# Optimization experiments

Hardware: AMD Instinct MI355X
Metric: run time of the kernel (lower is better)

## Reference

```python
import jax, jax.numpy as jnp
import numpy as np

N, G, MAX_N, E, H = 20000, 200, 100, 320000, 4
F_IN, NHID, NCLS = 128, 128, 10
DQ = 2 * NHID   # pooling-stack input dim = 2*nhid
K1 = 25         # ceil(0.25 * avg_num_nodes)


def _lin(key, fi, fo):
    kw, kb = jax.random.split(key)
    s = 1.0 / np.sqrt(fi)
    return (jax.random.uniform(kw, (fi, fo), jnp.float32, -s, s),
            jax.random.uniform(kb, (fo,), jnp.float32, -s, s))


def setup_inputs():
    key = jax.random.key(0)
    ks = jax.random.split(key, 32)
    x = jax.random.normal(ks[0], (N, F_IN), jnp.float32)
    gid = jax.random.randint(ks[1], (E,), 0, G)
    u = jax.random.randint(ks[2], (E,), 0, MAX_N)
    v = jax.random.randint(ks[3], (E,), 0, MAX_N)
    edge_index = jnp.stack([gid * MAX_N + u, gid * MAX_N + v]).astype(jnp.int32)
    batch = (jnp.arange(N) // MAX_N).astype(jnp.int32)
    d = {}
    d['x'], d['edge_index'], d['batch'] = x, edge_index, batch
    d['W1'], d['b1'] = _lin(ks[4], F_IN, NHID)
    d['W2'], d['b2'] = _lin(ks[5], NHID, NHID)
    d['S0'] = jax.random.normal(ks[6], (1, K1, DQ), jnp.float32) * (1.0 / np.sqrt(DQ))
    d['Wq0'], d['bq0'] = _lin(ks[7], DQ, DQ)
    d['Wk0'], d['bk0'] = _lin(ks[8], DQ, DQ)
    d['Wv0'], d['bv0'] = _lin(ks[9], DQ, DQ)
    d['Wo0'], d['bo0'] = _lin(ks[10], DQ, DQ)
    d['Wq1'], d['bq1'] = _lin(ks[11], DQ, NHID)
    d['Wk1'], d['bk1'] = _lin(ks[12], DQ, NHID)
    d['Wv1'], d['bv1'] = _lin(ks[13], DQ, NHID)
    d['Wo1'], d['bo1'] = _lin(ks[14], NHID, NHID)
    d['S2'] = jax.random.normal(ks[15], (1, 1, NHID), jnp.float32) * (1.0 / np.sqrt(NHID))
    d['Wq2'], d['bq2'] = _lin(ks[16], NHID, NHID)
    d['Wk2'], d['bk2'] = _lin(ks[17], NHID, NHID)
    d['Wv2'], d['bv2'] = _lin(ks[18], NHID, NHID)
    d['Wo2'], d['bo2'] = _lin(ks[19], NHID, NHID)
    d['Wl'], d['bl'] = _lin(ks[20], NHID, NHID)
    d['Wc1'], d['bc1'] = _lin(ks[21], NHID, NHID)
    d['Wc2'], d['bc2'] = _lin(ks[22], NHID, NHID // 2)
    d['Wc3'], d['bc3'] = _lin(ks[23], NHID // 2, NCLS)
    return d


def gcn(h, src, dst, W, b):
    # PyG GCNConv: add self loops, sym-normalize, scatter-add, bias
    h = h @ W
    loop = jnp.arange(N, dtype=src.dtype)
    s = jnp.concatenate([src, loop])
    t = jnp.concatenate([dst, loop])
    deg = jax.ops.segment_sum(jnp.ones(s.shape[0], h.dtype), t, num_segments=N)
    dinv = jax.lax.rsqrt(jnp.maximum(deg, 1.0))
    norm = (dinv[s] * dinv[t])[:, None]
    return jax.ops.segment_sum(h[s] * norm, t, num_segments=N) + b


def to_dense(v, batch):
    counts = jax.ops.segment_sum(jnp.ones(v.shape[0], jnp.int32), batch, num_segments=G)
    start = jnp.cumsum(counts) - counts
    pos = jnp.arange(v.shape[0]) - start[batch]
    dense = jnp.zeros((G, MAX_N, v.shape[1]), v.dtype).at[batch, pos].set(v)
    mask = jnp.zeros((G, MAX_N), bool).at[batch, pos].set(True)
    return dense, mask


def attn_block(Q, K, V, Wo, bo, mask_bias):
    # MAB core with cluster=True: softmax over the QUERY (seed) axis, ln=False
    B, nq, dv = Q.shape
    dh = dv // H
    Qh = Q.reshape(B, nq, H, dh)
    Kh = K.reshape(B, K.shape[1], H, dh)
    Vh = V.reshape(B, V.shape[1], H, dh)
    score = jnp.einsum('bqhd,bkhd->bhqk', Qh, Kh) / jnp.sqrt(jnp.float32(dv))
    if mask_bias is not None:
        score = score + mask_bias[:, None, None, :]
    A = jax.nn.softmax(score, axis=2)  # cluster assignment over seeds
    O = Q + jnp.einsum('bhqk,bkhd->bqhd', A, Vh).reshape(B, nq, dv)
    return O + jax.nn.relu(O @ Wo + bo)


def reference(x, edge_index, batch, W1, b1, W2, b2, S0, Wq0, bq0, Wk0, bk0, Wv0, bv0, Wo0, bo0,
              Wq1, bq1, Wk1, bk1, Wv1, bv1, Wo1, bo1, S2, Wq2, bq2, Wk2, bk2, Wv2, bv2, Wo2, bo2,
              Wl, bl, Wc1, bc1, Wc2, bc2, Wc3, bc3):
    src, dst = edge_index[0], edge_index[1]
    x1 = jax.nn.relu(gcn(x, src, dst, W1, b1))
    x2 = jax.nn.relu(gcn(x1, src, dst, W2, b2))
    p1 = jax.ops.segment_sum(x1, batch, num_segments=G)  # global_add_pool
    p2 = jax.ops.segment_sum(x2, batch, num_segments=G)
    xcat = jnp.concatenate([x1, x2], axis=1)             # [N, 2*nhid]
    dense, mask = to_dense(xcat, batch)
    mask_bias = (1.0 - mask.astype(jnp.float32)) * -1e9
    # --- GMPool_G: PMA with GCNConv for K/V on the node graph ---
    Kd, _ = to_dense(gcn(xcat, src, dst, Wk0, bk0), batch)
    Vd, _ = to_dense(gcn(xcat, src, dst, Wv0, bv0), batch)
    Q0 = jnp.broadcast_to(S0, (G, K1, DQ)) @ Wq0 + bq0
    O0 = attn_block(Q0, Kd, Vd, Wo0, bo0, mask_bias)     # [G, 25, 256]
    # --- SelfAtt (SAB), mask consumed above ---
    Q1 = O0 @ Wq1 + bq1
    K1d = O0 @ Wk1 + bk1
    V1d = O0 @ Wv1 + bv1
    O1 = attn_block(Q1, K1d, V1d, Wo1, bo1, None)        # [G, 25, 128]
    # --- GMPool_I: PMA with 1 seed ---
    Q2 = jnp.broadcast_to(S2, (G, 1, NHID)) @ Wq2 + bq2
    K2d = O1 @ Wk2 + bk2
    V2d = O1 @ Wv2 + bv2
    O2 = attn_block(Q2, K2d, V2d, Wo2, bo2, None)        # [G, 1, 128]
    z = (O2 @ Wl + bl)[:, 0, :]
    z = jax.nn.relu(z @ Wc1 + bc1)                        # dropout = identity at eval
    z = jax.nn.relu(z @ Wc2 + bc2)
    logits = z @ Wc3 + bc3
    return (logits, p1, p2)
```

## Files before the change

### kernel.cpp

```cpp
#include <hip/hip_runtime.h>
#include <hip/hip_bf16.h>
#include <cstdint>
#include <cstddef>

typedef __hip_bfloat16 bf16;
typedef __attribute__((ext_vector_type(8))) short s16x8;
typedef __attribute__((ext_vector_type(4))) float f32x4;

#define MAXN 100
#define HH   4
#define FIN  128
#define KS1  25
#define GLDK 136

static inline int ceil_div(int a, int b){ return (a + b - 1) / b; }

__device__ inline short f2bf(float f){
  unsigned int u = __float_as_uint(f);
  u = (u + 0x7FFF + ((u >> 16) & 1)) >> 16;
  return (short)u;
}
__device__ inline float loadf(const void* s, size_t i, bool isbf){
  return isbf ? __bfloat162float(((const bf16*)s)[i]) : ((const float*)s)[i];
}
__device__ inline bool block_sniff(const void* x, int tid, int* flagS){
  if (tid < 64){
    unsigned short b = ((const unsigned short*)x)[2 * tid];
    float v = __uint_as_float(((unsigned)b) << 16);
    float a = fabsf(v);
    bool ok = (a >= 6.1e-5f && a <= 16384.f);
    unsigned long long m = __ballot(ok);
    if (tid == 0) *flagS = (__popcll(m) >= 32) ? 1 : 0;
  }
  __syncthreads();
  return *flagS != 0;
}

struct PrepBatch {
  const void* src[40];
  void*       dst[40];
  int         a[40];
  int         b[40];
  int         blk0[41];
  int         ne;
  const void* xptr;
};

__global__ __launch_bounds__(256) void prep_all(PrepBatch pb){
  __shared__ int flagS;
  __shared__ short T[64][66];
  int tid = threadIdx.x;
  bool isbf = block_sniff(pb.xptr, tid, &flagS);
  int blk = blockIdx.x;
  int t = 0;
  while (t + 1 < pb.ne && pb.blk0[t + 1] <= blk) t++;
  int local = blk - pb.blk0[t];
  const void* s = pb.src[t];
  int bt = pb.b[t];
  if (bt < 0){
    float val = (bt == -2) ? 1.0f : 0.0f;
    int n = pb.a[t];
    float* d = (float*)pb.dst[t];
    int v = local * 256 + tid;
    int base = v * 4;
    if (base + 3 < n) ((float4*)d)[v] = make_float4(val, val, val, val);
    else for (int j = base; j < n && j < base + 4; j++) d[j] = val;
  } else if (bt == 0){
    int n = pb.a[t];
    float* d = (float*)pb.dst[t];
    int v = local * 256 + tid;
    int base = v * 4;
    if (base + 3 < n){
      float4 f;
      if (isbf){
        ushort4 u = ((const ushort4*)s)[v];
        f.x = __uint_as_float(((unsigned)u.x) << 16);
        f.y = __uint_as_float(((unsigned)u.y) << 16);
        f.z = __uint_as_float(((unsigned)u.z) << 16);
        f.w = __uint_as_float(((unsigned)u.w) << 16);
      } else f = ((const float4*)s)[v];
      ((float4*)d)[v] = f;
    } else {
      for (int j = base; j < n && j < base + 4; j++) d[j] = loadf(s, j, isbf);
    }
  } else {
    int K = pb.a[t], Nn = bt, ldt = K + 8;
    short* d = (short*)pb.dst[t];
    int tilesN = Nn >> 6;
    int tk = local / tilesN, tn = local - tk * tilesN;
    int k0 = tk << 6, n0 = tn << 6;
    int r = tid >> 6, c = tid & 63;
#pragma unroll
    for (int i = 0; i < 16; i++){
      int lk = r * 16 + i;
      T[lk][c] = f2bf(loadf(s, (size_t)(k0 + lk) * Nn + n0 + c, isbf));
    }
    __syncthreads();
#pragma unroll
    for (int i = 0; i < 16; i++){
      int ln = r * 16 + i;
      d[(size_t)(n0 + ln) * ldt + k0 + c] = T[c][ln];
    }
  }
}

__global__ __launch_bounds__(256) void adj_cnt(const int* __restrict__ src, const int* __restrict__ dst,
                                               float* __restrict__ A, int e){
  int i = blockIdx.x * 256 + threadIdx.x;
  if (i >= e) return;
  int s = src[i], d = dst[i];
  int g = d / MAXN;
  int dl = d - g * MAXN;
  int sl = s - (s / MAXN) * MAXN;
  atomicAdd(&A[(size_t)g * (MAXN * MAXN) + dl * MAXN + sl], 1.0f);
}

__global__ __launch_bounds__(256) void ubar_q0(const float* __restrict__ S0,
    const float* __restrict__ Wq0, const float* __restrict__ bq0,
    const float* __restrict__ Wk0, const float* __restrict__ bk0,
    float* __restrict__ Q0, short* __restrict__ Ubart, float* __restrict__ cvec)
{
  __shared__ float part[256];
  __shared__ float q0s[64];
  int j = blockIdx.x, h = j / 25, q = j - h * 25;
  int tid = threadIdx.x;
  {
    int c = tid & 63, kq = tid >> 6;
    const float* s0 = S0 + q * 256 + kq * 64;
    const float* wq = Wq0 + (size_t)(kq * 64) * 256 + h * 64 + c;
    float a = 0.f;
#pragma unroll
    for (int e = 0; e < 64; e++) a = fmaf(s0[e], wq[(size_t)e * 256], a);
    part[kq * 64 + c] = a;
  }
  __syncthreads();
  if (tid < 64){
    int c = h * 64 + tid;
    float acc = bq0[c] + part[tid] + part[64 + tid] + part[128 + tid] + part[192 + tid];
    q0s[tid] = acc;
    Q0[q * 256 + c] = acc;
  }
  __syncthreads();
  float acc = 0.f;
  const float* wp = &Wk0[(size_t)tid * 256 + h * 64];
#pragma unroll
  for (int d = 0; d < 64; d += 4){
    float4 w4 = *reinterpret_cast<const float4*>(wp + d);
    float4 q4 = *reinterpret_cast<const float4*>(&q0s[d]);
    acc = fmaf(w4.x, q4.x, acc); acc = fmaf(w4.y, q4.y, acc);
    acc = fmaf(w4.z, q4.z, acc); acc = fmaf(w4.w, q4.w, acc);
  }
  Ubart[(size_t)j * 264 + tid] = f2bf(acc * 0.0625f);
  if (tid == 0){
    float cb = 0.f;
    for (int d = 0; d < 64; d++) cb = fmaf(bk0[h * 64 + d], q0s[d], cb);
    cvec[j] = cb * 0.0625f;
  }
}

struct GTParams {
  const void* X;
  const float* Adj;
  const short* W1t; const float* b1;
  const short* W2t; const float* b2;
  float* p1; float* p2;
  const short* Wv0t;
  const short* Ubart;
  const float* biasVS;
  const float* Q0;
  const short* Wo0t;  const float* bo0;
  const short* WQKVt; const float* biasQKV;
  const short* Wo1t;  const float* bo1;
  const float *S2w, *Wq2, *bq2, *Wv2, *bv2, *Wo2, *bo2, *Wl, *bl, *Wc1, *bc1, *Wc2, *bc2, *Wc3, *bc3;
  float* out;
};

__global__ __launch_bounds__(512) void gcn_tail(GTParams P)
{
  __shared__ __align__(16) char pool[162880];
  __shared__ float dinvL[112];
  __shared__ int flagS;
  short* S1x = (short*)(pool);
  short* S2b = (short*)(pool + 30464);
  short* S4b = (short*)(pool + 65280);
  short* Asb = (short*)(pool + 100096);
  float* AdjL = (float*)(pool + 30464);
  char* R1 = pool;
  char* RV = pool + 57344;
  char* RS = pool + 122880;
  float* Ssh  = (float*)RS;
  short* Pbf  = (short*)R1;
  short* Abf  = (short*)(R1 + 34816);
  float* hva  = (float*)(R1 + 51712);
  float* hvb  = (float*)(R1 + 52224);
  float* O1F  = (float*)R1;
  float* OaF  = (float*)RS;
  float* ObF  = (float*)RS;
  short* Abf2 = (short*)(RS + 26000);
  float* QKV  = (float*)RV;
  float* Ss2  = (float*)(RV + 38800);
  float* hpart= (float*)(RV + 38800);

  int g = blockIdx.x, tid = threadIdx.x;
  bool isbf = block_sniff(P.X, tid, &flagS);
  int wave = tid >> 6, lane = tid & 63, quad = lane >> 4, l16 = lane & 15;
  int gn = wave * 16 + l16;

  s16x8 w1f[4], w2f[4];
#pragma unroll
  for (int kt = 0; kt < 4; kt++){
    int kb = kt * 32 + quad * 8;
    w1f[kt] = *reinterpret_cast<const s16x8*>(P.W1t + (size_t)gn * 136 + kb);
    w2f[kt] = *reinterpret_cast<const s16x8*>(P.W2t + (size_t)gn * 136 + kb);
  }

  for (int i = tid; i < 162880 / 4; i += 512) ((int*)pool)[i] = 0;
  __syncthreads();

  {
    const float* Ag = P.Adj + (size_t)g * (MAXN * MAXN);
    for (int i = tid; i < 2500; i += 512)
      ((float4*)AdjL)[i] = ((const float4*)Ag)[i];
  }
  for (int i = tid; i < MAXN * 16; i += 512){
    int r = i >> 4, k8 = (i & 15) << 3;
    s16x8 v;
    if (isbf){
      v = *reinterpret_cast<const s16x8*>((const short*)P.X + (size_t)(g * MAXN + r) * 128 + k8);
    } else {
      const float* ap = (const float*)P.X + (size_t)(g * MAXN + r) * 128 + k8;
      float4 f0 = *reinterpret_cast<const float4*>(ap);
      float4 f1 = *reinterpret_cast<const float4*>(ap + 4);
      v[0] = f2bf(f0.x); v[1] = f2bf(f0.y); v[2] = f2bf(f0.z); v[3] = f2bf(f0.w);
      v[4] = f2bf(f1.x); v[5] = f2bf(f1.y); v[6] = f2bf(f1.z); v[7] = f2bf(f1.w);
    }
    *reinterpret_cast<s16x8*>(&S1x[r * GLDK + k8]) = v;
  }
  __syncthreads();

  if (tid < 400){
    int r = tid >> 2, j0 = (tid & 3) * 25;
    const float* row = AdjL + r * 100 + j0;
    float s = 0.f;
#pragma unroll
    for (int j = 0; j < 25; j++) s += row[j];
    s += __shfl_xor(s, 1); s += __shfl_xor(s, 2);
    if ((tid & 3) == 0) dinvL[r] = rsqrtf(1.0f + s);
  }
  __syncthreads();

  for (int i = tid; i < MAXN * MAXN; i += 512){
    int r = i / MAXN, s = i - r * MAXN;
    float v = AdjL[i] + (r == s ? 1.0f : 0.0f);
    Asb[r * GLDK + s] = f2bf(v * dinvL[r] * dinvL[s]);
  }
  __syncthreads();

  f32x4 acc[7];
  auto zacc = [&](){
#pragma unroll
    for (int rt = 0; rt < 7; rt++) acc[rt] = (f32x4){0.f,0.f,0.f,0.f};
  };
  auto passL = [&](const short* Abuf, const short* Bbuf){
#pragma unroll
    for (int kt = 0; kt < 4; kt++){
      int kb = kt * 32 + quad * 8;
      s16x8 bf0 = *reinterpret_cast<const s16x8*>(&Bbuf[gn * GLDK + kb]);
#pragma unroll
      for (int rt = 0; rt < 7; rt++){
        s16x8 a = *reinterpret_cast<const s16x8*>(&Abuf[(rt * 16 + l16) * GLDK + kb]);
        acc[rt] = __builtin_amdgcn_mfma_f32_16x16x32_bf16(a, bf0, acc[rt], 0, 0, 0);
      }
    }
  };
  auto passGF = [&](const short* Abuf, const s16x8* bfr){
#pragma unroll
    for (int kt = 0; kt < 4; kt++){
      int kb = kt * 32 + quad * 8;
#pragma unroll
      for (int rt = 0; rt < 7; rt++){
        s16x8 a = *reinterpret_cast<const s16x8*>(&Abuf[(rt * 16 + l16) * GLDK + kb]);
        acc[rt] = __builtin_amdgcn_mfma_f32_16x16x32_bf16(a, bfr[kt], acc[rt], 0, 0, 0);
      }
    }
  };
  auto writeB = [&](short* Bbuf){
#pragma unroll
    for (int rt = 0; rt < 7; rt++){
      short4 o;
      o.x = f2bf(acc[rt][0]); o.y = f2bf(acc[rt][1]);
      o.z = f2bf(acc[rt][2]); o.w = f2bf(acc[rt][3]);
      *reinterpret_cast<short4*>(&Bbuf[gn * GLDK + rt * 16 + quad * 4]) = o;
    }
  };
  float s1sum = 0.f, s2sum = 0.f;
  auto hopEpi = [&](const float* bias, short* AoutA, short* BoutB, float& sum){
    float bv = bias[gn];
#pragma unroll
    for (int rt = 0; rt < 7; rt++){
      float vals[4];
#pragma unroll
      for (int r = 0; r < 4; r++){
        int row = rt * 16 + quad * 4 + r;
        float v = fmaxf(acc[rt][r] + bv, 0.f);
        vals[r] = v;
        if (row < MAXN) sum += v;
      }
      short4 o;
      o.x = f2bf(vals[0]); o.y = f2bf(vals[1]); o.z = f2bf(vals[2]); o.w = f2bf(vals[3]);
      *reinterpret_cast<short4*>(&BoutB[gn * GLDK + rt * 16 + quad * 4]) = o;
      if (AoutA){
        AoutA[(rt * 16 + quad * 4 + 0) * GLDK + gn] = o.x;
        AoutA[(rt * 16 + quad * 4 + 1) * GLDK + gn] = o.y;
        AoutA[(rt * 16 + quad * 4 + 2) * GLDK + gn] = o.z;
        AoutA[(rt * 16 + quad * 4 + 3) * GLDK + gn] = o.w;
      }
    }
  };

  zacc(); passGF(S1x, w1f); writeB(S2b);
  __syncthreads();
  zacc(); passL(Asb, S2b); hopEpi(P.b1, S1x, S4b, s1sum);
  __syncthreads();
  short4 xag0[7];
  zacc(); passL(Asb, S4b);
#pragma unroll
  for (int rt = 0; rt < 7; rt++){
    xag0[rt].x = f2bf(acc[rt][0]); xag0[rt].y = f2bf(acc[rt][1]);
    xag0[rt].z = f2bf(acc[rt][2]); xag0[rt].w = f2bf(acc[rt][3]);
  }
  zacc(); passGF(S1x, w2f); writeB(S2b);
  __syncthreads();
  zacc(); passL(Asb, S2b); hopEpi(P.b2, nullptr, S4b, s2sum);
  __syncthreads();
  zacc(); passL(Asb, S4b);

  s16x8 wvf[2][8], ubf[8];
  {
#pragma unroll
    for (int cg = 0; cg < 2; cg++){
      int c = wave * 32 + cg * 16 + l16;
      const short* bw = P.Wv0t + (size_t)c * 264;
#pragma unroll
      for (int kt = 0; kt < 8; kt++) wvf[cg][kt] = *reinterpret_cast<const s16x8*>(bw + kt * 32 + quad * 8);
    }
    int jj = (wave < 7) ? (wave * 16 + l16) : l16;
    const short* bw = P.Ubart + (size_t)jj * 264;
#pragma unroll
    for (int kt = 0; kt < 8; kt++) ubf[kt] = *reinterpret_cast<const s16x8*>(bw + kt * 32 + quad * 8);
  }

  s1sum += __shfl_xor(s1sum, 16); s1sum += __shfl_xor(s1sum, 32);
  s2sum += __shfl_xor(s2sum, 16); s2sum += __shfl_xor(s2sum, 32);
  if (quad == 0){
    P.p1[g * 128 + gn] = s1sum;
    P.p2[g * 128 + gn] = s2sum;
  }
  __syncthreads();

  {
    short v0[4];
#pragma unroll
    for (int rt = 0; rt < 7; rt++){
      v0[0] = xag0[rt].x; v0[1] = xag0[rt].y; v0[2] = xag0[rt].z; v0[3] = xag0[rt].w;
#pragma unroll
      for (int r = 0; r < 4; r++){
        int node = rt * 16 + quad * 4 + r;
        if (node < MAXN){
          int sw = (node & 7) << 4;
          *(short*)(R1 + ((node * 512 + gn * 2) ^ sw)) = v0[r];
          *(short*)(R1 + ((node * 512 + (gn + 128) * 2) ^ sw)) = f2bf(acc[rt][r]);
        }
      }
    }
    for (int i = tid; i < 1536; i += 512) ((int*)(R1 + 51200))[i] = 0;
  }
  __syncthreads();

  {
#pragma unroll
    for (int cg = 0; cg < 2; cg++){
      int c = wave * 32 + cg * 16 + l16;
      f32x4 vac[7];
#pragma unroll
      for (int rt = 0; rt < 7; rt++) vac[rt] = (f32x4){0.f,0.f,0.f,0.f};
#pragma unroll
      for (int kt = 0; kt < 8; kt++){
        int kb = kt * 32 + quad * 8;
#pragma unroll
        for (int rt = 0; rt < 7; rt++){
          int row = rt * 16 + l16;
          int ab = (row * 512 + kb * 2) ^ ((row & 7) << 4);
          s16x8 a = *reinterpret_cast<const s16x8*>(R1 + ab);
          vac[rt] = __builtin_amdgcn_mfma_f32_16x16x32_bf16(a, wvf[cg][kt], vac[rt], 0, 0, 0);
        }
      }
      float bv = P.biasVS[c];
#pragma unroll
      for (int rt = 0; rt < 7; rt++){
        int node0 = rt * 16 + quad * 4;
        short4 o;
        o.x = f2bf(vac[rt][0] + bv); o.y = f2bf(vac[rt][1] + bv);
        o.z = f2bf(vac[rt][2] + bv); o.w = f2bf(vac[rt][3] + bv);
        int b = (c * 256 + node0 * 2) ^ ((c & 7) << 4);
        *reinterpret_cast<short4*>(RV + b) = o;
      }
    }
    if (wave < 7){
      int j = wave * 16 + l16;
      f32x4 sac[7];
#pragma unroll
      for (int rt = 0; rt < 7; rt++) sac[rt] = (f32x4){0.f,0.f,0.f,0.f};
#pragma unroll
      for (int kt = 0; kt < 8; kt++){
        int kb = kt * 32 + quad * 8;
#pragma unroll
        for (int rt = 0; rt < 7; rt++){
          int row = rt * 16 + l16;
          int ab = (row * 512 + kb * 2) ^ ((row & 7) << 4);
          s16x8 a = *reinterpret_cast<const s16x8*>(R1 + ab);
          sac[rt] = __builtin_amdgcn_mfma_f32_16x16x32_bf16(a, ubf[kt], sac[rt], 0, 0, 0);
        }
      }
      if (j < 100){
        float cv = P.biasVS[256 + j];
#pragma unroll
        for (int rt = 0; rt < 7; rt++){
#pragma unroll
          for (int r = 0; r < 4; r++){
            int node = rt * 16 + quad * 4 + r;
            if (node < MAXN) Ssh[node * 100 + j] = sac[rt][r] + cv;
          }
        }
      }
    }
  }
  __syncthreads();

  if (tid < 400){
    int k = tid >> 2, h = tid & 3;
    const float* base = &Ssh[k * 100 + h * 25];
    float v[25];
    float m = -1e30f;
#pragma unroll
    for (int q = 0; q < 25; q++){ v[q] = base[q]; m = fmaxf(m, v[q]); }
    float s = 0.f;
#pragma unroll
    for (int q = 0; q < 25; q++){ float e = __expf(v[q] - m); v[q] = e; s += e; }
    float inv = 1.0f / s;
    short* pb = &Pbf[h * 32 * 136 + k];
#pragma unroll
    for (int q = 0; q < 25; q++) pb[q * 136] = f2bf(v[q] * inv);
  } else {
    for (int idx = tid - 400; idx < 1400; idx += 112){
      int r = idx / 14, c = idx - r * 14;
      int h = r / 25, q = r - h * 25;
      ((int*)Pbf)[(h * 32 + q) * 68 + 50 + c] = 0;
    }
  }
  __syncthreads();

  {
    int h = wave >> 1;
    int cbase = wave * 32;
    f32x4 aac[2][2];
#pragma unroll
    for (int rt = 0; rt < 2; rt++){ aac[rt][0] = (f32x4){0.f,0.f,0.f,0.f}; aac[rt][1] = aac[rt][0]; }
#pragma unroll
    for (int kt = 0; kt < 4; kt++){
      int kb = kt * 32 + quad * 8;
      int c0 = cbase + l16, c1 = cbase + 16 + l16;
      int b0 = (c0 * 256 + kb * 2) ^ ((c0 & 7) << 4);
      int b1 = (c1 * 256 + kb * 2) ^ ((c1 & 7) << 4);
      s16x8 vb0 = *reinterpret_cast<const s16x8*>(RV + b0);
      s16x8 vb1 = *reinterpret_cast<const s16x8*>(RV + b1);
#pragma unroll
      for (int rt = 0; rt < 2; rt++){
        s16x8 a = *reinterpret_cast<const s16x8*>(&Pbf[(h * 32 + rt * 16 + l16) * 136 + kb]);
        aac[rt][0] = __builtin_amdgcn_mfma_f32_16x16x32_bf16(a, vb0, aac[rt][0], 0, 0, 0);
        aac[rt][1] = __builtin_amdgcn_mfma_f32_16x16x32_bf16(a, vb1, aac[rt][1], 0, 0, 0);
      }
    }
    s16x8 o0f0[8], o0f1[8];
    {
      int c0w = wave * 16 + l16, c1w = c0w + 128;
#pragma unroll
      for (int kt = 0; kt < 8; kt++){
        int kb = kt * 32 + quad * 8;
        o0f0[kt] = *reinterpret_cast<const s16x8*>(&P.Wo0t[(size_t)c0w * 264 + kb]);
        o0f1[kt] = *reinterpret_cast<const s16x8*>(&P.Wo0t[(size_t)c1w * 264 + kb]);
      }
    }
#pragma unroll
    for (int cg = 0; cg < 2; cg++){
      int c = cbase + cg * 16 + l16;
#pragma unroll
      for (int rt = 0; rt < 2; rt++){
#pragma unroll
        for (int r = 0; r < 4; r++){
          int row = rt * 16 + quad * 4 + r;
          if (row < 25){
            float oa = aac[rt][cg][r] + P.Q0[row * 256 + c];
            OaF[row * 260 + c] = oa;
            Abf[row * 264 + c] = f2bf(oa);
          }
        }
      }
    }
    __syncthreads();

    {
      int c0 = wave * 16 + l16, c1 = c0 + 128;
      f32x4 a0[2], a1[2];
#pragma unroll
      for (int rt = 0; rt < 2; rt++){ a0[rt] = (f32x4){0.f,0.f,0.f,0.f}; a1[rt] = a0[rt]; }
#pragma unroll
      for (int kt = 0; kt < 8; kt++){
        int kb = kt * 32 + quad * 8;
#pragma unroll
        for (int rt = 0; rt < 2; rt++){
          s16x8 a = *reinterpret_cast<const s16x8*>(&Abf[(rt * 16 + l16) * 264 + kb]);
          a0[rt] = __builtin_amdgcn_mfma_f32_16x16x32_bf16(a, o0f0[kt], a0[rt], 0, 0, 0);
          a1[rt] = __builtin_amdgcn_mfma_f32_16x16x32_bf16(a, o0f1[kt], a1[rt], 0, 0, 0);
        }
      }
      __syncthreads();
#pragma unroll
      for (int cg = 0; cg < 2; cg++){
        int col = cg ? c1 : c0;
        float bv = P.bo0[col];
#pragma unroll
        for (int rt = 0; rt < 2; rt++){
          f32x4 av = cg ? a1[rt] : a0[rt];
#pragma unroll
          for (int r = 0; r < 4; r++){
            int row = rt * 16 + quad * 4 + r;
            if (row < 25){
              float t = av[r] + bv;
              Abf[row * 264 + col] = f2bf(OaF[row * 260 + col] + fmaxf(t, 0.f));
            }
          }
        }
      }
    }
  }
  s16x8 qkvf[3][8];
  {
    int c0 = wave * 16 + l16;
#pragma unroll
    for (int p2 = 0; p2 < 3; p2++)
#pragma unroll
      for (int kt = 0; kt < 8; kt++){
        int kb = kt * 32 + quad * 8;
        qkvf[p2][kt] = *reinterpret_cast<const s16x8*>(&P.WQKVt[(size_t)(c0 + p2 * 128) * 264 + kb]);
      }
  }
  __syncthreads();

  {
    int c0 = wave * 16 + l16;
    f32x4 qac[3][2];
#pragma unroll
    for (int p2 = 0; p2 < 3; p2++)
#pragma unroll
      for (int rt = 0; rt < 2; rt++) qac[p2][rt] = (f32x4){0.f,0.f,0.f,0.f};
#pragma unroll
    for (int kt = 0; kt < 8; kt++){
      int kb = kt * 32 + quad * 8;
#pragma unroll
      for (int rt = 0; rt < 2; rt++){
        s16x8 a = *reinterpret_cast<const s16x8*>(&Abf[(rt * 16 + l16) * 264 + kb]);
#pragma unroll
        for (int p2 = 0; p2 < 3; p2++)
          qac[p2][rt] = __builtin_amdgcn_mfma_f32_16x16x32_bf16(a, qkvf[p2][kt], qac[p2][rt], 0, 0, 0);
      }
    }
#pragma unroll
    for (int p2 = 0; p2 < 3; p2++){
      int col = c0 + p2 * 128;
      float bv = P.biasQKV[col];
#pragma unroll
      for (int rt = 0; rt < 2; rt++){
#pragma unroll
        for (int r = 0; r < 4; r++){
          int row = rt * 16 + quad * 4 + r;
          if (row < 25) QKV[row * 388 + col] = qac[p2][rt][r] + bv;
        }
      }
    }
  }
  __syncthreads();

  for (int idx = tid; idx < 2500; idx += 512){
    int h = idx / 625;
    int r = idx - h * 625;
    int q = r / 25, k = r - q * 25;
    const float* qp = &QKV[q * 388 + h * 32];
    const float* kp = &QKV[k * 388 + 128 + h * 32];
    float sac = 0.f;
#pragma unroll
    for (int d = 0; d < 32; d += 4){
      float4 a4 = *reinterpret_cast<const float4*>(&qp[d]);
      float4 b4 = *reinterpret_cast<const float4*>(&kp[d]);
      sac = fmaf(a4.x, b4.x, sac); sac = fmaf(a4.y, b4.y, sac);
      sac = fmaf(a4.z, b4.z, sac); sac = fmaf(a4.w, b4.w, sac);
    }
    Ss2[(h * 25 + q) * 26 + k] = sac * 0.0883883476f;
  }
  __syncthreads();
  if (tid < 100){
    int h = tid / 25, k = tid - h * 25;
    float m = -1e30f;
#pragma unroll
    for (int q = 0; q < 25; q++) m = fmaxf(m, Ss2[(h * 25 + q) * 26 + k]);
    float s = 0.f;
#pragma unroll
    for (int q = 0; q < 25; q++){ float e = __expf(Ss2[(h * 25 + q) * 26 + k] - m); Ss2[(h * 25 + q) * 26 + k] = e; s += e; }
    float inv = 1.0f / s;
#pragma unroll
    for (int q = 0; q < 25; q++) Ss2[(h * 25 + q) * 26 + k] *= inv;
  }
  __syncthreads();

  if (tid < 256){
    int qh = tid >> 7;
    int c = tid & 127, h = c >> 5;
    int q0 = qh * 13, nq = 13 - qh;
    float oac[13] = {};
    for (int k = 0; k < 25; k++){
      float v = QKV[k * 388 + 256 + c];
      for (int j = 0; j < nq; j++)
        oac[j] = fmaf(Ss2[(h * 25 + q0 + j) * 26 + k], v, oac[j]);
    }
    for (int j = 0; j < nq; j++){
      int q = q0 + j;
      float ob = QKV[q * 388 + c] + oac[j];
      ObF[q * 132 + c] = ob;
      Abf2[q * 136 + c] = f2bf(ob);
    }
  }
  s16x8 o1f[4];
  {
    int c0 = wave * 16 + l16;
#pragma unroll
    for (int kt = 0; kt < 4; kt++){
      int kb = kt * 32 + quad * 8;
      o1f[kt] = *reinterpret_cast<const s16x8*>(&P.Wo1t[(size_t)c0 * 136 + kb]);
    }
  }
  __syncthreads();

  {
    int c0 = wave * 16 + l16;
    f32x4 a0 = (f32x4){0.f,0.f,0.f,0.f}, a1 = a0;
#pragma unroll
    for (int kt = 0; kt < 4; kt++){
      int kb = kt * 32 + quad * 8;
      s16x8 aA = *reinterpret_cast<const s16x8*>(&Abf2[l16 * 136 + kb]);
      s16x8 aB = *reinterpret_cast<const s16x8*>(&Abf2[(16 + l16) * 136 + kb]);
      a0 = __builtin_amdgcn_mfma_f32_16x16x32_bf16(aA, o1f[kt], a0, 0, 0, 0);
      a1 = __builtin_amdgcn_mfma_f32_16x16x32_bf16(aB, o1f[kt], a1, 0, 0, 0);
    }
    float bv = P.bo1[c0];
#pragma unroll
    for (int r = 0; r < 4; r++){
      int row0 = quad * 4 + r;
      if (row0 < 25){ float t = a0[r] + bv; O1F[row0 * 132 + c0] = ObF[row0 * 132 + c0] + fmaxf(t, 0.f); }
      int row1 = 16 + quad * 4 + r;
      if (row1 < 25){ float t = a1[r] + bv; O1F[row1 * 132 + c0] = ObF[row1 * 132 + c0] + fmaxf(t, 0.f); }
    }
  }
  __syncthreads();

  if (tid < 128){
    float s = 0.f;
    for (int k = 0; k < 25; k++) s += O1F[k * 132 + tid];
    hva[tid] = s;
  }
  __syncthreads();
  {
    int kh = tid >> 7, c = tid & 127, k0 = kh * 32;
    float s = 0.f;
    for (int k = k0; k < k0 + 32; k++)
      s = fmaf(P.S2w[k], P.Wq2[k * 128 + c], fmaf(hva[k], P.Wv2[k * 128 + c], s));
    hpart[kh * 128 + c] = s;
    __syncthreads();
    if (tid < 128) hvb[c] = hpart[c] + hpart[128 + c] + hpart[256 + c] + hpart[384 + c]
                          + P.bq2[c] + 25.f * P.bv2[c];
    __syncthreads();
    s = 0.f;
    for (int k = k0; k < k0 + 32; k++) s = fmaf(hvb[k], P.Wo2[k * 128 + c], s);
    hpart[kh * 128 + c] = s;
    __syncthreads();
    if (tid < 128) hva[c] = hvb[c] + fmaxf(hpart[c] + hpart[128 + c] + hpart[256 + c] + hpart[384 + c] + P.bo2[c], 0.f);
    __syncthreads();
    s = 0.f;
    for (int k = k0; k < k0 + 32; k++) s = fmaf(hva[k], P.Wl[k * 128 + c], s);
    hpart[kh * 128 + c] = s;
    __syncthreads();
    if (tid < 128) hvb[c] = hpart[c] + hpart[128 + c] + hpart[256 + c] + hpart[384 + c] + P.bl[c];
    __syncthreads();
    s = 0.f;
    for (int k = k0; k < k0 + 32; k++) s = fmaf(hvb[k], P.Wc1[k * 128 + c], s);
    hpart[kh * 128 + c] = s;
    __syncthreads();
    if (tid < 128) hva[c] = fmaxf(hpart[c] + hpart[128 + c] + hpart[256 + c] + hpart[384 + c] + P.bc1[c], 0.f);
    __syncthreads();
    {
      int kh2 = tid >> 6, c2 = tid & 63, kk0 = kh2 * 16;
      float s2 = 0.f;
      for (int k = kk0; k < kk0 + 16; k++) s2 = fmaf(hva[k], P.Wc2[k * 64 + c2], s2);
      hpart[kh2 * 64 + c2] = s2;
    }
    __syncthreads();
    if (tid < 64){
      float s2 = hpart[tid] + hpart[64 + tid] + hpart[128 + tid] + hpart[192 + tid]
               + hpart[256 + tid] + hpart[320 + tid] + hpart[384 + tid] + hpart[448 + tid];
      hvb[tid] = fmaxf(s2 + P.bc2[tid], 0.f);
    }
    __syncthreads();
    if (tid < 10){
      float lg = P.bc3[tid];
      for (int k = 0; k < 64; k++) lg = fmaf(hvb[k], P.Wc3[k * 10 + tid], lg);
      P.out[g * 10 + tid] = lg;
    }
  }
}

extern "C" void kernel_launch(void* const* d_in, const int* in_sizes, int n_in,
                              void* d_out, int out_size, void* d_ws, size_t ws_size,
                              hipStream_t stream)
{
  const int*  edge = (const int*)d_in[1];
  const int N = in_sizes[0] / FIN;
  const int E = in_sizes[1] / 2;
  const int G = N / MAXN;
  const int* srcp = edge;
  const int* dstp = edge + E;
  float* out = (float*)d_out;

  float* w = (float*)d_ws;
  size_t off = 0;
  auto alloc = [&](size_t nfl){ nfl = (nfl + 3) & ~(size_t)3; float* p = w + off; off += nfl; return p; };
  auto allocS = [&](size_t nsh)->short*{ size_t nfl = ((nsh + 1) / 2 + 3) & ~(size_t)3; short* p = (short*)(w + off); off += nfl; return p; };

  float* biasVS  = alloc(356);
  float* biasQKV = alloc(384);
  float* cvec = biasVS + 256;

  const int castT[24] = {4,6,7,8,9,10,11,15,23,24,25,26,29,30,31,32,33,34,35,36,37,38,39,40};
  float* wf[41] = {nullptr};
  for (int i = 0; i < 24; i++) wf[castT[i]] = alloc((size_t)in_sizes[castT[i]]);
  wf[13] = biasVS; wf[17] = biasQKV; wf[19] = biasQKV + 128; wf[21] = biasQKV + 256;

  float* Adj = alloc((size_t)G * MAXN * MAXN);
  float* Q0  = alloc(25 * 256);

  short* W1t   = allocS(128 * 136);
  short* W2t   = allocS(128 * 136);
  short* WVSt  = allocS(356 * 264);
  short* WQKVt = allocS(384 * 264);
  short* Wo0t  = allocS(256 * 264);
  short* Wo1t  = allocS(128 * 136);
  short* Ubart = WVSt + (size_t)256 * 264;
  if (off * sizeof(float) > ws_size) return;

  dim3 blk(256);

  PrepBatch pb; int ne = 0, blks = 0;
  pb.xptr = d_in[0];
  auto addC = [&](const void* s, float* d, int n){
    pb.src[ne]=s; pb.dst[ne]=d; pb.a[ne]=n; pb.b[ne]=0; pb.blk0[ne]=blks;
    blks += ceil_div(ceil_div(n, 4), 256); ne++; };
  auto addW = [&](const void* s, short* d, int K, int Nn){
    pb.src[ne]=s; pb.dst[ne]=d; pb.a[ne]=K; pb.b[ne]=Nn; pb.blk0[ne]=blks;
    blks += (K >> 6) * (Nn >> 6); ne++; };
  auto addF = [&](void* d, int n, int mode){
    pb.src[ne]=nullptr; pb.dst[ne]=d; pb.a[ne]=n; pb.b[ne]=mode; pb.blk0[ne]=blks;
    blks += ceil_div(ceil_div(n, 4), 256); ne++; };
  for (int i = 0; i < 24; i++){ int t = castT[i]; addC(d_in[t], wf[t], in_sizes[t]); }
  addC(d_in[13], biasVS, 256);
  addC(d_in[17], biasQKV, 128); addC(d_in[19], biasQKV + 128, 128); addC(d_in[21], biasQKV + 256, 128);
  addW(d_in[3],  W1t, 128, 128);             addW(d_in[5],  W2t, 128, 128);
  addW(d_in[12], WVSt, 256, 256);            addW(d_in[16], WQKVt, 256, 128);
  addW(d_in[18], WQKVt + 128*264, 256, 128); addW(d_in[20], WQKVt + 256*264, 256, 128);
  addW(d_in[14], Wo0t, 256, 256);            addW(d_in[22], Wo1t, 128, 128);
  addF(Adj, G * MAXN * MAXN, -1);
  pb.blk0[ne] = blks; pb.ne = ne;
  prep_all<<<dim3(blks), blk, 0, stream>>>(pb);

  adj_cnt<<<ceil_div(E, 256), blk, 0, stream>>>(srcp, dstp, Adj, E);

  ubar_q0<<<dim3(100), blk, 0, stream>>>(wf[7], wf[8], wf[9], wf[10], wf[11], Q0, Ubart, cvec);

  GTParams tp;
  tp.X = d_in[0]; tp.Adj = Adj;
  tp.W1t = W1t; tp.b1 = wf[4]; tp.W2t = W2t; tp.b2 = wf[6];
  tp.p1 = out + 2000; tp.p2 = out + 27600;
  tp.Wv0t = WVSt; tp.Ubart = Ubart; tp.biasVS = biasVS;
  tp.Q0 = Q0;
  tp.Wo0t = Wo0t; tp.bo0 = wf[15];
  tp.WQKVt = WQKVt; tp.biasQKV = biasQKV;
  tp.Wo1t = Wo1t; tp.bo1 = wf[23];
  tp.S2w = wf[24]; tp.Wq2 = wf[25]; tp.bq2 = wf[26]; tp.Wv2 = wf[29]; tp.bv2 = wf[30];
  tp.Wo2 = wf[31]; tp.bo2 = wf[32]; tp.Wl = wf[33]; tp.bl = wf[34];
  tp.Wc1 = wf[35]; tp.bc1 = wf[36]; tp.Wc2 = wf[37]; tp.bc2 = wf[38];
  tp.Wc3 = wf[39]; tp.bc3 = wf[40];
  tp.out = out;
  gcn_tail<<<dim3(G), dim3(512), 0, stream>>>(tp);
}
```

Baseline: 232.9 us.

## Fold edge-count scatter into prep kernel, memset adjacency, use LDS-only barriers

The adjacency zero-fill moves out of the prep kernel into a hipMemsetAsync. The separate adj_cnt launch is folded into prep_all as extra blocks, which saves one kernel launch. Inside gcn_tail, every __syncthreads becomes a barrier that waits only on LDS counters (lgkmcnt), not on outstanding global memory operations. That avoids draining vector memory loads at each barrier, but it is only correct if nothing after a barrier depends on global stores or loads issued before it.

Measured after the change: 224.5 us, median of 2. -3.6%, faster.

```diff
diff --git a/kernel.cpp b/kernel.cpp
--- a/kernel.cpp
+++ b/kernel.cpp
@@ -22,6 +22,10 @@
 }
 __device__ inline float loadf(const void* s, size_t i, bool isbf){
   return isbf ? __bfloat162float(((const bf16*)s)[i]) : ((const float*)s)[i];
+}
+__device__ inline void barrier_lds(){
+  asm volatile("s_waitcnt lgkmcnt(0)" ::: "memory");
+  __builtin_amdgcn_s_barrier();
 }
 __device__ inline bool block_sniff(const void* x, int tid, int* flagS){
   if (tid < 64){
@@ -43,29 +47,36 @@
   int         b[40];
   int         blk0[41];
   int         ne;
+  int         nTaskBlks;
   const void* xptr;
+  const int *esrc, *edst; float* eadj; int ecnt;
 };
 
 __global__ __launch_bounds__(256) void prep_all(PrepBatch pb){
   __shared__ int flagS;
   __shared__ short T[64][66];
   int tid = threadIdx.x;
+  int blk = blockIdx.x;
+
+  if (blk >= pb.nTaskBlks){
+    int i = (blk - pb.nTaskBlks) * 256 + tid;
+    if (i < pb.ecnt){
+      int s = pb.esrc[i], d = pb.edst[i];
+      int g = d / MAXN;
+      int dl = d - g * MAXN;
+      int sl = s - (s / MAXN) * MAXN;
+      atomicAdd(&pb.eadj[(size_t)g * (MAXN * MAXN) + dl * MAXN + sl], 1.0f);
+    }
+    return;
+  }
+
   bool isbf = block_sniff(pb.xptr, tid, &flagS);
-  int blk = blockIdx.x;
   int t = 0;
   while (t + 1 < pb.ne && pb.blk0[t + 1] <= blk) t++;
   int local = blk - pb.blk0[t];
   const void* s = pb.src[t];
   int bt = pb.b[t];
-  if (bt < 0){
-    float val = (bt == -2) ? 1.0f : 0.0f;
-    int n = pb.a[t];
-    float* d = (float*)pb.dst[t];
-    int v = local * 256 + tid;
-    int base = v * 4;
-    if (base + 3 < n) ((float4*)d)[v] = make_float4(val, val, val, val);
-    else for (int j = base; j < n && j < base + 4; j++) d[j] = val;
-  } else if (bt == 0){
+  if (bt == 0){
     int n = pb.a[t];
     float* d = (float*)pb.dst[t];
     int v = local * 256 + tid;
@@ -102,17 +113,6 @@
       d[(size_t)(n0 + ln) * ldt + k0 + c] = T[c][ln];
     }
   }
-}
-
-__global__ __launch_bounds__(256) void adj_cnt(const int* __restrict__ src, const int* __restrict__ dst,
-                                               float* __restrict__ A, int e){
-  int i = blockIdx.x * 256 + threadIdx.x;
-  if (i >= e) return;
-  int s = src[i], d = dst[i];
-  int g = d / MAXN;
-  int dl = d - g * MAXN;
-  int sl = s - (s / MAXN) * MAXN;
-  atomicAdd(&A[(size_t)g * (MAXN * MAXN) + dl * MAXN + sl], 1.0f);
 }
 
 __global__ __launch_bounds__(256) void ubar_q0(const float* __restrict__ S0,
@@ -215,7 +215,7 @@
   }
 
   for (int i = tid; i < 162880 / 4; i += 512) ((int*)pool)[i] = 0;
-  __syncthreads();
+  barrier_lds();
 
   {
     const float* Ag = P.Adj + (size_t)g * (MAXN * MAXN);
@@ -236,7 +236,7 @@
     }
     *reinterpret_cast<s16x8*>(&S1x[r * GLDK + k8]) = v;
   }
-  __syncthreads();
+  barrier_lds();
 
   if (tid < 400){
     int r = tid >> 2, j0 = (tid & 3) * 25;
@@ -247,14 +247,14 @@
     s += __shfl_xor(s, 1); s += __shfl_xor(s, 2);
     if ((tid & 3) == 0) dinvL[r] = rsqrtf(1.0f + s);
   }
-  __syncthreads();
+  barrier_lds();
 
   for (int i = tid; i < MAXN * MAXN; i += 512){
     int r = i / MAXN, s = i - r * MAXN;
     float v = AdjL[i] + (r == s ? 1.0f : 0.0f);
     Asb[r * GLDK + s] = f2bf(v * dinvL[r] * dinvL[s]);
   }
-  __syncthreads();
+  barrier_lds();
 
   f32x4 acc[7];
   auto zacc = [&](){
@@ -319,9 +319,9 @@
   };
 
   zacc(); passGF(S1x, w1f); writeB(S2b);
-  __syncthreads();
+  barrier_lds();
   zacc(); passL(Asb, S2b); hopEpi(P.b1, S1x, S4b, s1sum);
-  __syncthreads();
+  barrier_lds();
   short4 xag0[7];
   zacc(); passL(Asb, S4b);
 #pragma unroll
@@ -330,9 +330,9 @@
     xag0[rt].z = f2bf(acc[rt][2]); xag0[rt].w = f2bf(acc[rt][3]);
   }
   zacc(); passGF(S1x, w2f); writeB(S2b);
-  __syncthreads();
+  barrier_lds();
   zacc(); passL(Asb, S2b); hopEpi(P.b2, nullptr, S4b, s2sum);
-  __syncthreads();
+  barrier_lds();
   zacc(); passL(Asb, S4b);
 
   s16x8 wvf[2][8], ubf[8];
@@ -356,7 +356,7 @@
     P.p1[g * 128 + gn] = s1sum;
     P.p2[g * 128 + gn] = s2sum;
   }
-  __syncthreads();
+  barrier_lds();
 
   {
     short v0[4];
@@ -375,7 +375,7 @@
     }
     for (int i = tid; i < 1536; i += 512) ((int*)(R1 + 51200))[i] = 0;
   }
-  __syncthreads();
+  barrier_lds();
 
   {
 #pragma unroll
@@ -435,7 +435,7 @@
       }
     }
   }
-  __syncthreads();
+  barrier_lds();
 
   if (tid < 400){
     int k = tid >> 2, h = tid & 3;
@@ -458,7 +458,7 @@
       ((int*)Pbf)[(h * 32 + q) * 68 + 50 + c] = 0;
     }
   }
-  __syncthreads();
+  barrier_lds();
 
   {
     int h = wave >> 1;
@@ -507,7 +507,7 @@
         }
       }
     }
-    __syncthreads();
+    barrier_lds();
 
     {
       int c0 = wave * 16 + l16, c1 = c0 + 128;
@@ -524,7 +524,7 @@
           a1[rt] = __builtin_amdgcn_mfma_f32_16x16x32_bf16(a, o0f1[kt], a1[rt], 0, 0, 0);
         }
       }
-      __syncthreads();
+      barrier_lds();
 #pragma unroll
       for (int cg = 0; cg < 2; cg++){
         int col = cg ? c1 : c0;
@@ -555,7 +555,7 @@
         qkvf[p2][kt] = *reinterpret_cast<const s16x8*>(&P.WQKVt[(size_t)(c0 + p2 * 128) * 264 + kb]);
       }
   }
-  __syncthreads();
+  barrier_lds();
 
   {
     int c0 = wave * 16 + l16;
@@ -589,7 +589,7 @@
       }
     }
   }
-  __syncthreads();
+  barrier_lds();
 
   for (int idx = tid; idx < 2500; idx += 512){
     int h = idx / 625;
@@ -607,7 +607,7 @@
     }
     Ss2[(h * 25 + q) * 26 + k] = sac * 0.0883883476f;
   }
-  __syncthreads();
+  barrier_lds();
   if (tid < 100){
     int h = tid / 25, k = tid - h * 25;
     float m = -1e30f;
@@ -620,7 +620,7 @@
 #pragma unroll
     for (int q = 0; q < 25; q++) Ss2[(h * 25 + q) * 26 + k] *= inv;
   }
-  __syncthreads();
+  barrier_lds();
 
   if (tid < 256){
     int qh = tid >> 7;
@@ -648,7 +648,7 @@
       o1f[kt] = *reinterpret_cast<const s16x8*>(&P.Wo1t[(size_t)c0 * 136 + kb]);
     }
   }
-  __syncthreads();
+  barrier_lds();
 
   {
     int c0 = wave * 16 + l16;
@@ -670,55 +670,55 @@
       if (row1 < 25){ float t = a1[r] + bv; O1F[row1 * 132 + c0] = ObF[row1 * 132 + c0] + fmaxf(t, 0.f); }
     }
   }
-  __syncthreads();
+  barrier_lds();
 
   if (tid < 128){
     float s = 0.f;
     for (int k = 0; k < 25; k++) s += O1F[k * 132 + tid];
     hva[tid] = s;
   }
-  __syncthreads();
+  barrier_lds();
   {
     int kh = tid >> 7, c = tid & 127, k0 = kh * 32;
     float s = 0.f;
     for (int k = k0; k < k0 + 32; k++)
       s = fmaf(P.S2w[k], P.Wq2[k * 128 + c], fmaf(hva[k], P.Wv2[k * 128 + c], s));
     hpart[kh * 128 + c] = s;
-    __syncthreads();
+    barrier_lds();
     if (tid < 128) hvb[c] = hpart[c] + hpart[128 + c] + hpart[256 + c] + hpart[384 + c]
                           + P.bq2[c] + 25.f * P.bv2[c];
-    __syncthreads();
+    barrier_lds();
     s = 0.f;
     for (int k = k0; k < k0 + 32; k++) s = fmaf(hvb[k], P.Wo2[k * 128 + c], s);
     hpart[kh * 128 + c] = s;
-    __syncthreads();
+    barrier_lds();
     if (tid < 128) hva[c] = hvb[c] + fmaxf(hpart[c] + hpart[128 + c] + hpart[256 + c] + hpart[384 + c] + P.bo2[c], 0.f);
-    __syncthreads();
+    barrier_lds();
     s = 0.f;
     for (int k = k0; k < k0 + 32; k++) s = fmaf(hva[k], P.Wl[k * 128 + c], s);
     hpart[kh * 128 + c] = s;
-    __syncthreads();
+    barrier_lds();
     if (tid < 128) hvb[c] = hpart[c] + hpart[128 + c] + hpart[256 + c] + hpart[384 + c] + P.bl[c];
-    __syncthreads();
+    barrier_lds();
     s = 0.f;
     for (int k = k0; k < k0 + 32; k++) s = fmaf(hvb[k], P.Wc1[k * 128 + c], s);
     hpart[kh * 128 + c] = s;
-    __syncthreads();
+    barrier_lds();
     if (tid < 128) hva[c] = fmaxf(hpart[c] + hpart[128 + c] + hpart[256 + c] + hpart[384 + c] + P.bc1[c], 0.f);
-    __syncthreads();
+    barrier_lds();
     {
       int kh2 = tid >> 6, c2 = tid & 63, kk0 = kh2 * 16;
       float s2 = 0.f;
       for (int k = kk0; k < kk0 + 16; k++) s2 = fmaf(hva[k], P.Wc2[k * 64 + c2], s2);
       hpart[kh2 * 64 + c2] = s2;
     }
-    __syncthreads();
+    barrier_lds();
     if (tid < 64){
       float s2 = hpart[tid] + hpart[64 + tid] + hpart[128 + tid] + hpart[192 + tid]
                + hpart[256 + tid] + hpart[320 + tid] + hpart[384 + tid] + hpart[448 + tid];
       hvb[tid] = fmaxf(s2 + P.bc2[tid], 0.f);
     }
-    __syncthreads();
+    barrier_lds();
     if (tid < 10){
       float lg = P.bc3[tid];
       for (int k = 0; k < 64; k++) lg = fmaf(hvb[k], P.Wc3[k * 10 + tid], lg);
@@ -767,6 +767,8 @@
 
   dim3 blk(256);
 
+  (void)hipMemsetAsync(Adj, 0, (size_t)G * MAXN * MAXN * sizeof(float), stream);
+
   PrepBatch pb; int ne = 0, blks = 0;
   pb.xptr = d_in[0];
   auto addC = [&](const void* s, float* d, int n){
@@ -775,9 +777,6 @@
   auto addW = [&](const void* s, short* d, int K, int Nn){
     pb.src[ne]=s; pb.dst[ne]=d; pb.a[ne]=K; pb.b[ne]=Nn; pb.blk0[ne]=blks;
     blks += (K >> 6) * (Nn >> 6); ne++; };
-  auto addF = [&](void* d, int n, int mode){
-    pb.src[ne]=nullptr; pb.dst[ne]=d; pb.a[ne]=n; pb.b[ne]=mode; pb.blk0[ne]=blks;
-    blks += ceil_div(ceil_div(n, 4), 256); ne++; };
   for (int i = 0; i < 24; i++){ int t = castT[i]; addC(d_in[t], wf[t], in_sizes[t]); }
   addC(d_in[13], biasVS, 256);
   addC(d_in[17], biasQKV, 128); addC(d_in[19], biasQKV + 128, 128); addC(d_in[21], biasQKV + 256, 128);
@@ -785,11 +784,11 @@
   addW(d_in[12], WVSt, 256, 256);            addW(d_in[16], WQKVt, 256, 128);
   addW(d_in[18], WQKVt + 128*264, 256, 128); addW(d_in[20], WQKVt + 256*264, 256, 128);
   addW(d_in[14], Wo0t, 256, 256);            addW(d_in[22], Wo1t, 128, 128);
-  addF(Adj, G * MAXN * MAXN, -1);
   pb.blk0[ne] = blks; pb.ne = ne;
-  prep_all<<<dim3(blks), blk, 0, stream>>>(pb);
-
-  adj_cnt<<<ceil_div(E, 256), blk, 0, stream>>>(srcp, dstp, Adj, E);
+  pb.nTaskBlks = blks;
+  pb.esrc = srcp; pb.edst = dstp; pb.eadj = Adj; pb.ecnt = E;
+  int nEdgeBlks = ceil_div(E, 256);
+  prep_all<<<dim3(blks + nEdgeBlks), blk, 0, stream>>>(pb);
 
   ubar_q0<<<dim3(100), blk, 0, stream>>>(wf[7], wf[8], wf[9], wf[10], wf[11], Q0, Ubart, cvec);
 
```
